# Optimization experiments

Hardware: AMD Instinct MI355X
Metric: run time of the kernel (lower is better)

The kernel has to match this reference:

```python
import jax, jax.numpy as jnp
import numpy as np

LMBDA = 0.4            # trade-off between relevance and xQuAD diversity weight
HEAD_TAIL_SPLIT = 280  # number of most-popular items forming the 'head' category
NEG = -10000.0         # score assigned to already-observed (train) items
U, I = 2048, 25000


def setup_inputs() -> dict:
    key = jax.random.key(0)
    k1, k2, k3 = jax.random.split(key, 3)
    predicted_relevance = jax.random.normal(k1, (U, I), dtype=jnp.float32)
    observed_relevance = (jax.random.uniform(k2, (U, I)) < 0.02).astype(jnp.float32)
    item_popularity = jax.random.uniform(k3, (I,), dtype=jnp.float32)
    return {
        "predicted_relevance": predicted_relevance,
        "observed_relevance": observed_relevance,
        "item_popularity": item_popularity,
        "k": 10,
        "rmax": 100,
    }


def reference(predicted_relevance, observed_relevance, item_popularity, k, rmax):
    n_items = item_popularity.shape[0]
    # head/tail split by popularity rank (argsort descending, top head_tail_split = head)
    order = jnp.argsort(-item_popularity)
    head_mask = jnp.zeros(n_items, jnp.float32).at[order[:HEAD_TAIL_SPLIT]].set(1.0)

    def rerank_user(scores, obs):
        # min-max normalize user scores, then suppress train items
        s = (scores - scores.min()) / (scores.max() - scores.min())
        s = jnp.where(obs > 0, NEG, s)
        # p(d|u): fraction of user's observed interactions in head vs tail
        obs_sum = jnp.sum(obs)
        p_head = jnp.sum(obs * head_mask) / obs_sum
        p_tail = 1.0 - p_head
        # candidate pool: rmax most relevant items
        cand_vals, cand_idx = jax.lax.top_k(s, rmax)  # [rmax]
        cand_head = head_mask[cand_idx]               # 1.0 if candidate in head

        def step(carry, t):
            sel_mask, c_head, n_sel = carry
            denom = jnp.maximum(n_sel, 1.0)
            # smooth xQuAD redundancy factor: 1 - (#selected in category)/|S|; 1 when S empty
            f_head = jnp.where(n_sel > 0, 1.0 - c_head / denom, 1.0)
            f_tail = jnp.where(n_sel > 0, 1.0 - (n_sel - c_head) / denom, 1.0)
            w = p_head * cand_head * f_head + p_tail * (1.0 - cand_head) * f_tail
            comb = (1.0 - LMBDA) * cand_vals + LMBDA * w
            comb = jnp.where(sel_mask, -jnp.inf, comb)  # suppress already-picked candidates
            best = jnp.argmax(comb)
            item = cand_idx[best]
            is_head = cand_head[best]
            new_carry = (sel_mask.at[best].set(True), c_head + is_head, n_sel + 1.0)
            val = (k - (t + 1.0)) / k  # rank-based relevance written back
            return new_carry, (item, val)

        carry0 = (jnp.zeros(rmax, dtype=bool), jnp.float32(0.0), jnp.float32(0.0))
        _, (items, vals) = jax.lax.scan(step, carry0, jnp.arange(k, dtype=jnp.float32))
        return jnp.zeros_like(scores).at[items].set(vals)

    return jax.vmap(rerank_user)(predicted_relevance, observed_relevance)
```

## Files before the change

kernel.cpp:

```cpp
#include <hip/hip_runtime.h>
#include <math.h>

#define NITEMS 25000
#define NF4    6250
#define NHW    782
#define HEADN  280
#define KSEL   10
#define RMAX   100
#define HBINS  2048
#define CBINS  256
#define PCAP   1024
#define CCAP   512
#define THRESH 1.9f
#define BLK    512
#define NWAVE  (BLK/64)
#define HBLK   1024
#define ZGRID  2048

typedef float vfloat4 __attribute__((ext_vector_type(4)));

template<int OP, int NW>
__device__ __forceinline__ float blk_reduce(float v, float* scratch, int tid) {
#pragma unroll
  for (int o = 1; o < 64; o <<= 1) {
    float t = __shfl_xor(v, o);
    if (OP == 0) v = fminf(v, t);
    else if (OP == 1) v = fmaxf(v, t);
    else v += t;
  }
  if ((tid & 63) == 0) scratch[tid >> 6] = v;
  __syncthreads();
  float r = scratch[0];
#pragma unroll
  for (int w = 1; w < NW; ++w) {
    float t = scratch[w];
    if (OP == 0) r = fminf(r, t);
    else if (OP == 1) r = fmaxf(r, t);
    else r += t;
  }
  __syncthreads();
  return r;
}

template<int NB>
__device__ __forceinline__ int find_boundary_wave0(const int* hist, int thr, int tid) {
  const int CH = NB / 64;
  int lc = 0;
#pragma unroll
  for (int j = 0; j < CH; ++j) lc += hist[tid * CH + j];
  int s = lc;
#pragma unroll
  for (int o = 1; o < 64; o <<= 1) {
    int t = __shfl_down(s, o);
    if (tid + o < 64) s += t;
  }
  unsigned long long m = __ballot(s >= thr);
  int cstar = 63 - __clzll(m);
  int nl = cstar + 1; if (nl > 63) nl = 63;
  int sn = __shfl(s, nl);
  if (cstar == 63) sn = 0;
  int bs = cstar * CH;
  if (tid == 0) {
    int acc = sn;
    for (int b = (cstar + 1) * CH - 1; b >= cstar * CH; --b) {
      acc += hist[b];
      if (acc >= thr) { bs = b; break; }
    }
  }
  bs = __shfl(bs, 0);
  return bs;
}

__global__ __launch_bounds__(HBLK) void zero_head_kernel(const float* __restrict__ pop,
                                                         unsigned int* __restrict__ hb,
                                                         vfloat4* __restrict__ out4,
                                                         int total4) {
  const int tid = threadIdx.x;
  if (blockIdx.x > 0) {
    int idx = ((int)blockIdx.x - 1) * HBLK + tid;
    const int stride = ZGRID * HBLK;
    const vfloat4 zz = (vfloat4)(0.f);
    for (; idx < total4; idx += stride) __builtin_nontemporal_store(zz, &out4[idx]);
    return;
  }
  __shared__ float sp[NITEMS];
  __shared__ int   s_hist[HBINS];
  __shared__ float s_red[HBLK / 64];
  __shared__ int   s_bstar, s_m;
  __shared__ int   s_bidx[1024];
  __shared__ unsigned int s_bits[NHW];

  for (int i = tid; i < NITEMS; i += HBLK) sp[i] = pop[i];
  for (int i = tid; i < HBINS; i += HBLK) s_hist[i] = 0;
  for (int i = tid; i < NHW; i += HBLK) s_bits[i] = 0u;
  if (tid == 0) s_m = 0;
  __syncthreads();

  for (int i = tid; i < NITEMS; i += HBLK) {
    int b = (int)(sp[i] * (float)HBINS);
    b = b < 0 ? 0 : (b > HBINS - 1 ? HBINS - 1 : b);
    atomicAdd(&s_hist[b], 1);
  }
  __syncthreads();

  if (tid < 64) {
    int bs = find_boundary_wave0<HBINS>(s_hist, HEADN, tid);
    if (tid == 0) s_bstar = bs;
  }
  __syncthreads();
  const int bstar = s_bstar;

  float a = 0.f;
  for (int b = tid; b < HBINS; b += HBLK) if (b > bstar) a += (float)s_hist[b];
  a = blk_reduce<2, HBLK / 64>(a, s_red, tid);
  const int A = (int)a;

  for (int i = tid; i < NITEMS; i += HBLK) {
    int b = (int)(sp[i] * (float)HBINS);
    b = b < 0 ? 0 : (b > HBINS - 1 ? HBINS - 1 : b);
    if (b > bstar) atomicOr(&s_bits[i >> 5], 1u << (i & 31));
    else if (b == bstar) {
      int p = atomicAdd(&s_m, 1);
      if (p < 1024) s_bidx[p] = i;
    }
  }
  __syncthreads();
  const int m = (s_m < 1024) ? s_m : 1024;

  for (int c = tid; c < m; c += HBLK) {
    int idx = s_bidx[c];
    float v = sp[idx];
    int r = A;
    for (int l = 0; l < m; ++l) {
      int il = s_bidx[l];
      float vl = sp[il];
      r += (vl > v || (vl == v && il < idx)) ? 1 : 0;
    }
    if (r < HEADN) atomicOr(&s_bits[idx >> 5], 1u << (idx & 31));
  }
  __syncthreads();
  for (int i = tid; i < NHW; i += HBLK) hb[i] = s_bits[i];
}

__device__ __forceinline__ int codeof(float v) {
  int b = (int)((v - 2.0f) * 64.0f);
  return b < 0 ? 0 : (b > CBINS - 1 ? CBINS - 1 : b);
}

__global__ __launch_bounds__(BLK, 4) void rerank_kernel(const float* __restrict__ pred,
                                                        const float* __restrict__ obs,
                                                        const unsigned int* __restrict__ hb,
                                                        float* __restrict__ out) {
  __shared__ unsigned int s_hb[NHW];
  __shared__ int   s_pi[PCAP];
  __shared__ float s_pv[PCAP];
  __shared__ int   s_hist[CBINS];
  __shared__ float s_red4[NWAVE * 4];
  __shared__ int   s_pn, s_C, s_bstar;
  __shared__ int   s_ci[CCAP];
  __shared__ float s_nv[CCAP];
  __shared__ float s_tv[RMAX];
  __shared__ int   s_tidx[RMAX];
  __shared__ float s_th[RMAX];
  __shared__ int   s_items[KSEL];

  const int tid = threadIdx.x;
  const int u = blockIdx.x;
  const vfloat4* __restrict__ p4 = (const vfloat4*)(pred + (size_t)u * NITEMS);
  const vfloat4* __restrict__ o4 = (const vfloat4*)(obs + (size_t)u * NITEMS);
  float* orow = out + (size_t)u * NITEMS;

  for (int i = tid; i < NHW; i += BLK) s_hb[i] = hb[i];
  if (tid == 0) { s_pn = 0; s_C = 0; }
  if (tid < CBINS) s_hist[tid] = 0;
  __syncthreads();

  float mn = INFINITY, mx = -INFINITY, osum = 0.f, ohead = 0.f;

#define PROC1(xx, oo, base)                                                        \
  do {                                                                             \
    float m4n = fminf(fminf(xx.x, xx.y), fminf(xx.z, xx.w));                       \
    float m4x = fmaxf(fmaxf(xx.x, xx.y), fmaxf(xx.z, xx.w));                       \
    mn = fminf(mn, m4n);                                                           \
    mx = fmaxf(mx, m4x);                                                           \
    float os4 = oo.x + oo.y + oo.z + oo.w;                     \
    osum += os4;                                                                   \
    if (os4 > 0.f) {                                                               \
      if (oo.x > 0.f) ohead += (float)((s_hb[((base)+0) >> 5] >> (((base)+0) & 31)) & 1u); \
      if (oo.y > 0.f) ohead += (float)((s_hb[((base)+1) >> 5] >> (((base)+1) & 31)) & 1u); \
      if (oo.z > 0.f) ohead += (float)((s_hb[((base)+2) >> 5] >> (((base)+2) & 31)) & 1u); \
      if (oo.w > 0.f) ohead += (float)((s_hb[((base)+3) >> 5] >> (((base)+3) & 31)) & 1u); \
    }                                                                              \
    if (m4x > THRESH) {                                                            \
      if (xx.x > THRESH && oo.x <= 0.f) { int p = atomicAdd(&s_pn, 1); if (p < PCAP) { s_pi[p] = (base)+0; s_pv[p] = xx.x; } } \
      if (xx.y > THRESH && oo.y <= 0.f) { int p = atomicAdd(&s_pn, 1); if (p < PCAP) { s_pi[p] = (base)+1; s_pv[p] = xx.y; } } \
      if (xx.z > THRESH && oo.z <= 0.f) { int p = atomicAdd(&s_pn, 1); if (p < PCAP) { s_pi[p] = (base)+2; s_pv[p] = xx.z; } } \
      if (xx.w > THRESH && oo.w <= 0.f) { int p = atomicAdd(&s_pn, 1); if (p < PCAP) { s_pi[p] = (base)+3; s_pv[p] = xx.w; } } \
    }                                                                              \
  } while (0)

  int i = tid;
  for (; i + 3 * BLK < NF4; i += 4 * BLK) {
    vfloat4 x0 = p4[i];
    vfloat4 x1 = p4[i + BLK];
    vfloat4 x2 = p4[i + 2 * BLK];
    vfloat4 x3 = p4[i + 3 * BLK];
    vfloat4 o0 = o4[i];
    vfloat4 o1 = o4[i + BLK];
    vfloat4 o2 = o4[i + 2 * BLK];
    vfloat4 o3 = o4[i + 3 * BLK];
    asm volatile("" : "+v"(x0), "+v"(x1), "+v"(x2), "+v"(x3),
                      "+v"(o0), "+v"(o1), "+v"(o2), "+v"(o3));
    PROC1(x0, o0, 4 * i);
    PROC1(x1, o1, 4 * (i + BLK));
    PROC1(x2, o2, 4 * (i + 2 * BLK));
    PROC1(x3, o3, 4 * (i + 3 * BLK));
  }
  for (; i < NF4; i += BLK) {
    vfloat4 xr = p4[i];
    vfloat4 orr = o4[i];
    PROC1(xr, orr, 4 * i);
  }
#undef PROC1

#pragma unroll
  for (int o = 1; o < 64; o <<= 1) {
    mn = fminf(mn, __shfl_xor(mn, o));
    mx = fmaxf(mx, __shfl_xor(mx, o));
    osum += __shfl_xor(osum, o);
    ohead += __shfl_xor(ohead, o);
  }
  if ((tid & 63) == 0) {
    int w = tid >> 6;
    s_red4[w * 4 + 0] = mn;  s_red4[w * 4 + 1] = mx;
    s_red4[w * 4 + 2] = osum; s_red4[w * 4 + 3] = ohead;
  }
  __syncthreads();
  mn = s_red4[0]; mx = s_red4[1]; osum = s_red4[2]; ohead = s_red4[3];
#pragma unroll
  for (int w = 1; w < NWAVE; ++w) {
    mn = fminf(mn, s_red4[w * 4 + 0]);
    mx = fmaxf(mx, s_red4[w * 4 + 1]);
    osum += s_red4[w * 4 + 2];
    ohead += s_red4[w * 4 + 3];
  }

  const float range  = __fsub_rn(mx, mn);
  const float p_head = __fdiv_rn(ohead, osum);
  const float p_tail = __fsub_rn(1.0f, p_head);
  const int pn = (s_pn < PCAP) ? s_pn : PCAP;

  for (int c = tid; c < pn; c += BLK) atomicAdd(&s_hist[codeof(s_pv[c])], 1);
  __syncthreads();

  if (tid < 64) {
    int bs = find_boundary_wave0<CBINS>(s_hist, RMAX, tid);
    if (tid == 0) s_bstar = (bs > 0) ? bs - 1 : 0;
  }
  __syncthreads();
  const int bcut = s_bstar;

  for (int c = tid; c < pn; c += BLK) {
    float v = s_pv[c];
    if (codeof(v) >= bcut) {
      int p = atomicAdd(&s_C, 1);
      if (p < CCAP) {
        s_ci[p] = s_pi[c];
        s_nv[p] = __fdiv_rn(__fsub_rn(v, mn), range);
      }
    }
  }
  __syncthreads();
  const int C = (s_C < CCAP) ? s_C : CCAP;

  for (int c = tid; c < C; c += BLK) {
    float n = s_nv[c]; int id = s_ci[c];
    int r = 0;
    for (int l = 0; l < C; ++l) {
      float nl = s_nv[l]; int il = s_ci[l];
      r += (nl > n || (nl == n && il < id)) ? 1 : 0;
    }
    if (r < RMAX) { s_tv[r] = n; s_tidx[r] = id; }
  }
  __syncthreads();
  if (tid < RMAX) {
    int id = s_tidx[tid];
    s_th[tid] = (float)((s_hb[id >> 5] >> (id & 31)) & 1u);
  }
  __syncthreads();

  if (tid < 64) {
    const int r0 = tid, r1 = tid + 64;
    bool sel0 = false, sel1 = false;
    const float v0 = (r0 < RMAX) ? s_tv[r0] : 0.f;
    const float h0 = (r0 < RMAX) ? s_th[r0] : 0.f;
    const float v1 = (r1 < RMAX) ? s_tv[r1] : 0.f;
    const float h1 = (r1 < RMAX) ? s_th[r1] : 0.f;
    float c_head = 0.f, n_sel = 0.f;
    for (int t = 0; t < KSEL; ++t) {
      float f_head = 1.0f, f_tail = 1.0f;
      if (n_sel > 0.f) {
        float denom = fmaxf(n_sel, 1.0f);
        f_head = __fsub_rn(1.0f, __fdiv_rn(c_head, denom));
        f_tail = __fsub_rn(1.0f, __fdiv_rn(__fsub_rn(n_sel, c_head), denom));
      }
      const float wh = __fmul_rn(p_head, f_head);
      const float wt = __fmul_rn(p_tail, f_tail);
      float comb0 = -INFINITY, comb1 = -INFINITY;
      if (r0 < RMAX && !sel0) {
        float w = (h0 > 0.5f) ? wh : wt;
        comb0 = __fadd_rn(__fmul_rn(0.6f, v0), __fmul_rn(0.4f, w));
      }
      if (r1 < RMAX && !sel1) {
        float w = (h1 > 0.5f) ? wh : wt;
        comb1 = __fadd_rn(__fmul_rn(0.6f, v1), __fmul_rn(0.4f, w));
      }
      float bv = (comb1 > comb0) ? comb1 : comb0;
      int   bi = (comb1 > comb0) ? r1 : r0;
#pragma unroll
      for (int o = 1; o < 64; o <<= 1) {
        float ov = __shfl_xor(bv, o);
        int   oi = __shfl_xor(bi, o);
        if (ov > bv || (ov == bv && oi < bi)) { bv = ov; bi = oi; }
      }
      const float bh = s_th[bi];
      if (tid == 0) s_items[t] = s_tidx[bi];
      if (bi == r0) sel0 = true;
      if (bi == r1) sel1 = true;
      c_head = c_head + bh;
      n_sel  = n_sel + 1.0f;
    }
  }
  __syncthreads();

  if (tid < KSEL) {
    float tf = (float)tid;
    float val = __fdiv_rn(__fsub_rn((float)KSEL, __fadd_rn(tf, 1.0f)), (float)KSEL);
    orow[s_items[tid]] = val;
  }
}

extern "C" void kernel_launch(void* const* d_in, const int* in_sizes, int n_in,
                              void* d_out, int out_size, void* d_ws, size_t ws_size,
                              hipStream_t stream) {
  const float* pred = (const float*)d_in[0];
  const float* obs  = (const float*)d_in[1];
  const float* pop  = (const float*)d_in[2];
  float* out = (float*)d_out;
  unsigned int* hb = (unsigned int*)d_ws;
  const int nusers = in_sizes[0] / NITEMS;
  const int total4 = nusers * NF4;

  hipLaunchKernelGGL(zero_head_kernel, dim3(1 + ZGRID), dim3(HBLK), 0, stream,
                     pop, hb, (vfloat4*)out, total4);
  hipLaunchKernelGGL(rerank_kernel, dim3(nusers), dim3(BLK), 0, stream, pred, obs, hb, out);
}
```

Baseline: 142.9 us.

## Gather head-item list to compute head observations instead of per-element bitmask lookups

The head kernel now also writes an explicit list of the 280 head item indices to the workspace. The rerank kernel drops its shared bitmask copy and the per-element observed-head checks in the streaming loop. Instead it gathers the user's observation values at the head indices after the stream, and reads head bits from global memory for the candidates. Other changes: nontemporal loads for predictions, removal of the asm register pin, and launch bounds raised to 8 blocks per CU. The extra gather is scattered and may hit the cache, and a higher occupancy target may cause register spills.

```diff
diff --git a/kernel.cpp b/kernel.cpp
--- a/kernel.cpp
+++ b/kernel.cpp
@@ -17,6 +17,9 @@
 #define HBLK   1024
 #define ZGRID  2048
 
+#define WS_HB    0
+#define WS_HIDX  1024
+
 typedef float vfloat4 __attribute__((ext_vector_type(4)));
 
 template<int OP, int NW>
@@ -72,7 +75,7 @@
 }
 
 __global__ __launch_bounds__(HBLK) void zero_head_kernel(const float* __restrict__ pop,
-                                                         unsigned int* __restrict__ hb,
+                                                         unsigned int* __restrict__ ws,
                                                          vfloat4* __restrict__ out4,
                                                          int total4) {
   const int tid = threadIdx.x;
@@ -86,14 +89,14 @@
   __shared__ float sp[NITEMS];
   __shared__ int   s_hist[HBINS];
   __shared__ float s_red[HBLK / 64];
-  __shared__ int   s_bstar, s_m;
+  __shared__ int   s_bstar, s_m, s_ln;
   __shared__ int   s_bidx[1024];
   __shared__ unsigned int s_bits[NHW];
 
   for (int i = tid; i < NITEMS; i += HBLK) sp[i] = pop[i];
   for (int i = tid; i < HBINS; i += HBLK) s_hist[i] = 0;
   for (int i = tid; i < NHW; i += HBLK) s_bits[i] = 0u;
-  if (tid == 0) s_m = 0;
+  if (tid == 0) { s_m = 0; s_ln = 0; }
   __syncthreads();
 
   for (int i = tid; i < NITEMS; i += HBLK) {
@@ -118,8 +121,11 @@
   for (int i = tid; i < NITEMS; i += HBLK) {
     int b = (int)(sp[i] * (float)HBINS);
     b = b < 0 ? 0 : (b > HBINS - 1 ? HBINS - 1 : b);
-    if (b > bstar) atomicOr(&s_bits[i >> 5], 1u << (i & 31));
-    else if (b == bstar) {
+    if (b > bstar) {
+      atomicOr(&s_bits[i >> 5], 1u << (i & 31));
+      int p = atomicAdd(&s_ln, 1);
+      if (p < HEADN) ws[WS_HIDX + p] = (unsigned int)i;
+    } else if (b == bstar) {
       int p = atomicAdd(&s_m, 1);
       if (p < 1024) s_bidx[p] = i;
     }
@@ -136,10 +142,14 @@
       float vl = sp[il];
       r += (vl > v || (vl == v && il < idx)) ? 1 : 0;
     }
-    if (r < HEADN) atomicOr(&s_bits[idx >> 5], 1u << (idx & 31));
-  }
-  __syncthreads();
-  for (int i = tid; i < NHW; i += HBLK) hb[i] = s_bits[i];
+    if (r < HEADN) {
+      atomicOr(&s_bits[idx >> 5], 1u << (idx & 31));
+      int p = atomicAdd(&s_ln, 1);
+      if (p < HEADN) ws[WS_HIDX + p] = (unsigned int)idx;
+    }
+  }
+  __syncthreads();
+  for (int i = tid; i < NHW; i += HBLK) ws[WS_HB + i] = s_bits[i];
 }
 
 __device__ __forceinline__ int codeof(float v) {
@@ -147,11 +157,10 @@
   return b < 0 ? 0 : (b > CBINS - 1 ? CBINS - 1 : b);
 }
 
-__global__ __launch_bounds__(BLK, 4) void rerank_kernel(const float* __restrict__ pred,
+__global__ __launch_bounds__(BLK, 8) void rerank_kernel(const float* __restrict__ pred,
                                                         const float* __restrict__ obs,
-                                                        const unsigned int* __restrict__ hb,
+                                                        const unsigned int* __restrict__ ws,
                                                         float* __restrict__ out) {
-  __shared__ unsigned int s_hb[NHW];
   __shared__ int   s_pi[PCAP];
   __shared__ float s_pv[PCAP];
   __shared__ int   s_hist[CBINS];
@@ -168,14 +177,14 @@
   const int u = blockIdx.x;
   const vfloat4* __restrict__ p4 = (const vfloat4*)(pred + (size_t)u * NITEMS);
   const vfloat4* __restrict__ o4 = (const vfloat4*)(obs + (size_t)u * NITEMS);
+  const float* __restrict__ obsrow = obs + (size_t)u * NITEMS;
   float* orow = out + (size_t)u * NITEMS;
 
-  for (int i = tid; i < NHW; i += BLK) s_hb[i] = hb[i];
   if (tid == 0) { s_pn = 0; s_C = 0; }
   if (tid < CBINS) s_hist[tid] = 0;
   __syncthreads();
 
-  float mn = INFINITY, mx = -INFINITY, osum = 0.f, ohead = 0.f;
+  float mn = INFINITY, mx = -INFINITY, osum = 0.f;
 
 #define PROC1(xx, oo, base)                                                        \
   do {                                                                             \
@@ -183,14 +192,7 @@
     float m4x = fmaxf(fmaxf(xx.x, xx.y), fmaxf(xx.z, xx.w));                       \
     mn = fminf(mn, m4n);                                                           \
     mx = fmaxf(mx, m4x);                                                           \
-    float os4 = oo.x + oo.y + oo.z + oo.w;                     \
-    osum += os4;                                                                   \
-    if (os4 > 0.f) {                                                               \
-      if (oo.x > 0.f) ohead += (float)((s_hb[((base)+0) >> 5] >> (((base)+0) & 31)) & 1u); \
-      if (oo.y > 0.f) ohead += (float)((s_hb[((base)+1) >> 5] >> (((base)+1) & 31)) & 1u); \
-      if (oo.z > 0.f) ohead += (float)((s_hb[((base)+2) >> 5] >> (((base)+2) & 31)) & 1u); \
-      if (oo.w > 0.f) ohead += (float)((s_hb[((base)+3) >> 5] >> (((base)+3) & 31)) & 1u); \
-    }                                                                              \
+    osum += oo.x + oo.y + oo.z + oo.w;                         \
     if (m4x > THRESH) {                                                            \
       if (xx.x > THRESH && oo.x <= 0.f) { int p = atomicAdd(&s_pn, 1); if (p < PCAP) { s_pi[p] = (base)+0; s_pv[p] = xx.x; } } \
       if (xx.y > THRESH && oo.y <= 0.f) { int p = atomicAdd(&s_pn, 1); if (p < PCAP) { s_pi[p] = (base)+1; s_pv[p] = xx.y; } } \
@@ -201,27 +203,31 @@
 
   int i = tid;
   for (; i + 3 * BLK < NF4; i += 4 * BLK) {
-    vfloat4 x0 = p4[i];
-    vfloat4 x1 = p4[i + BLK];
-    vfloat4 x2 = p4[i + 2 * BLK];
-    vfloat4 x3 = p4[i + 3 * BLK];
+    vfloat4 x0 = __builtin_nontemporal_load(&p4[i]);
+    vfloat4 x1 = __builtin_nontemporal_load(&p4[i + BLK]);
+    vfloat4 x2 = __builtin_nontemporal_load(&p4[i + 2 * BLK]);
+    vfloat4 x3 = __builtin_nontemporal_load(&p4[i + 3 * BLK]);
     vfloat4 o0 = o4[i];
     vfloat4 o1 = o4[i + BLK];
     vfloat4 o2 = o4[i + 2 * BLK];
     vfloat4 o3 = o4[i + 3 * BLK];
-    asm volatile("" : "+v"(x0), "+v"(x1), "+v"(x2), "+v"(x3),
-                      "+v"(o0), "+v"(o1), "+v"(o2), "+v"(o3));
     PROC1(x0, o0, 4 * i);
     PROC1(x1, o1, 4 * (i + BLK));
     PROC1(x2, o2, 4 * (i + 2 * BLK));
     PROC1(x3, o3, 4 * (i + 3 * BLK));
   }
   for (; i < NF4; i += BLK) {
-    vfloat4 xr = p4[i];
+    vfloat4 xr = __builtin_nontemporal_load(&p4[i]);
     vfloat4 orr = o4[i];
     PROC1(xr, orr, 4 * i);
   }
 #undef PROC1
+
+  float ohead = 0.f;
+  for (int j = tid; j < HEADN; j += BLK) {
+    int it = (int)ws[WS_HIDX + j];
+    ohead += (obsrow[it] > 0.f) ? 1.0f : 0.0f;
+  }
 
 #pragma unroll
   for (int o = 1; o < 64; o <<= 1) {
@@ -285,7 +291,7 @@
   __syncthreads();
   if (tid < RMAX) {
     int id = s_tidx[tid];
-    s_th[tid] = (float)((s_hb[id >> 5] >> (id & 31)) & 1u);
+    s_th[tid] = (float)((ws[WS_HB + (id >> 5)] >> (id & 31)) & 1u);
   }
   __syncthreads();
 
@@ -347,11 +353,11 @@
   const float* obs  = (const float*)d_in[1];
   const float* pop  = (const float*)d_in[2];
   float* out = (float*)d_out;
-  unsigned int* hb = (unsigned int*)d_ws;
+  unsigned int* ws = (unsigned int*)d_ws;
   const int nusers = in_sizes[0] / NITEMS;
   const int total4 = nusers * NF4;
 
   hipLaunchKernelGGL(zero_head_kernel, dim3(1 + ZGRID), dim3(HBLK), 0, stream,
-                     pop, hb, (vfloat4*)out, total4);
-  hipLaunchKernelGGL(rerank_kernel, dim3(nusers), dim3(BLK), 0, stream, pred, obs, hb, out);
-}
+                     pop, ws, (vfloat4*)out, total4);
+  hipLaunchKernelGGL(rerank_kernel, dim3(nusers), dim3(BLK), 0, stream, pred, obs, ws, out);
+}
```

After: 137.5 us. 1.04x faster.
